# Kernel optimization log

Hardware: AMD Instinct MI355X
Metric: run time of the kernel (lower is better)

## Reference

```python
import jax, jax.numpy as jnp
import numpy as np
import math

B, T, C, H = 2, 2048, 1024, 16
HD = C // H  # head dim = 64

def setup_inputs() -> dict:
    key = jax.random.key(0)
    ks = jax.random.split(key, 12)
    s = 0.02
    return {
        "x": jax.random.normal(ks[0], (B, T, C), dtype=jnp.float32),
        "ln1_g": jnp.ones((C,), jnp.float32),
        "ln1_b": jnp.zeros((C,), jnp.float32),
        "W_attn": jax.random.normal(ks[1], (C, 3 * C), jnp.float32) * s,
        "b_attn": jnp.zeros((3 * C,), jnp.float32),
        "W_ap": jax.random.normal(ks[2], (C, C), jnp.float32) * s,
        "b_ap": jnp.zeros((C,), jnp.float32),
        "ln2_g": jnp.ones((C,), jnp.float32),
        "ln2_b": jnp.zeros((C,), jnp.float32),
        "W_fc": jax.random.normal(ks[3], (C, 4 * C), jnp.float32) * s,
        "b_fc": jnp.zeros((4 * C,), jnp.float32),
        "W_mp": jax.random.normal(ks[4], (4 * C, C), jnp.float32) * s,
        "b_mp": jnp.zeros((C,), jnp.float32),
    }

def layernorm(x, g, b, eps=1e-5):
    mu = jnp.mean(x, axis=-1, keepdims=True)
    var = jnp.mean(jnp.square(x - mu), axis=-1, keepdims=True)
    return (x - mu) * jax.lax.rsqrt(var + eps) * g + b

def gelu_tanh(x):
    # GELU(approximate='tanh')
    c = math.sqrt(2.0 / math.pi)
    return 0.5 * x * (1.0 + jnp.tanh(c * (x + 0.044715 * x * x * x)))

def attention(x, W_attn, b_attn, W_ap, b_ap):
    b, t, c = x.shape
    qkv = x @ W_attn + b_attn                      # [B,T,3C]
    q, k, v = jnp.split(qkv, 3, axis=-1)
    q = q.reshape(b, t, H, HD).transpose(0, 2, 1, 3)  # [B,H,T,hd]
    k = k.reshape(b, t, H, HD).transpose(0, 2, 1, 3)
    v = v.reshape(b, t, H, HD).transpose(0, 2, 1, 3)
    attn = jnp.einsum('bhqd,bhkd->bhqk', q, k) * (1.0 / math.sqrt(HD))
    mask = jnp.tril(jnp.ones((t, t), dtype=bool))
    attn = jnp.where(mask, attn, jnp.float32(-jnp.inf))
    attn = jax.nn.softmax(attn, axis=-1)
    y = jnp.einsum('bhqk,bhkd->bhqd', attn, v)
    y = y.transpose(0, 2, 1, 3).reshape(b, t, c)
    return y @ W_ap + b_ap

def reference(x, ln1_g, ln1_b, W_attn, b_attn, W_ap, b_ap,
              ln2_g, ln2_b, W_fc, b_fc, W_mp, b_mp):
    x = x + attention(layernorm(x, ln1_g, ln1_b), W_attn, b_attn, W_ap, b_ap)
    h = layernorm(x, ln2_g, ln2_b)
    h = gelu_tanh(h @ W_fc + b_fc) @ W_mp + b_mp
    return x + h
```

## Files before the change

kernel.cpp:

```cpp
#include <hip/hip_runtime.h>
#include <stdint.h>

#define TT_ 2048
#define CC_ 1024

typedef unsigned short u16;
typedef __bf16 bf16x8 __attribute__((ext_vector_type(8)));
typedef __bf16 bf16x4 __attribute__((ext_vector_type(4)));
typedef float f32x4 __attribute__((ext_vector_type(4)));
typedef unsigned short u16x8 __attribute__((ext_vector_type(8)));

__device__ __forceinline__ u16 f2bf(float f) {
  unsigned u = __float_as_uint(f);
  u += 0x7fff + ((u >> 16) & 1);
  return (u16)(u >> 16);
}
__device__ __forceinline__ float bf2f(u16 v) {
  return __uint_as_float(((unsigned)v) << 16);
}

__device__ __forceinline__ float gelu_f(float t) {
  float u = 1.5957691216057308f * (t + 0.044715f * t * t * t);
  return t / (1.f + __expf(-u));
}

__device__ __forceinline__ void async_cp16(const u16* g, u16* l) {
  __builtin_amdgcn_global_load_lds(
      (const __attribute__((address_space(1))) void*)(uintptr_t)g,
      (__attribute__((address_space(3))) void*)(uint32_t)(uintptr_t)l,
      16, 0, 0);
}

__device__ __forceinline__ void blockbar() {
  asm volatile("" ::: "memory");
  __builtin_amdgcn_s_barrier();
  asm volatile("" ::: "memory");
}

__global__ __launch_bounds__(256) void kconv_t(const float* __restrict__ W,
                                               u16* __restrict__ WT, int K, int N) {
  __shared__ float t[32][33];
  int n0 = blockIdx.x * 32, k0 = blockIdx.y * 32;
  int tx = threadIdx.x & 31, ty = threadIdx.x >> 5;
#pragma unroll
  for (int r = 0; r < 4; ++r)
    t[ty + 8 * r][tx] = W[(size_t)(k0 + ty + 8 * r) * N + n0 + tx];
  __syncthreads();
#pragma unroll
  for (int r = 0; r < 4; ++r)
    WT[(size_t)(n0 + ty + 8 * r) * K + k0 + tx] = f2bf(t[tx][ty + 8 * r]);
}

__global__ __launch_bounds__(256) void kln(const float* __restrict__ x,
                                           const float* __restrict__ g,
                                           const float* __restrict__ b,
                                           u16* __restrict__ out) {
  int row = blockIdx.x, tid = threadIdx.x;
  const float4* xr = (const float4*)(x + (size_t)row * CC_);
  float4 v = xr[tid];
  float s = v.x + v.y + v.z + v.w;
  float s2 = v.x * v.x + v.y * v.y + v.z * v.z + v.w * v.w;
#pragma unroll
  for (int off = 32; off; off >>= 1) { s += __shfl_down(s, off); s2 += __shfl_down(s2, off); }
  __shared__ float rs[4], rq[4];
  int w = tid >> 6;
  if ((tid & 63) == 0) { rs[w] = s; rq[w] = s2; }
  __syncthreads();
  s = rs[0] + rs[1] + rs[2] + rs[3];
  s2 = rq[0] + rq[1] + rq[2] + rq[3];
  float mean = s * (1.f / CC_);
  float var = s2 * (1.f / CC_) - mean * mean;
  float rstd = rsqrtf(var + 1e-5f);
  float4 gv = ((const float4*)g)[tid];
  float4 bv = ((const float4*)b)[tid];
  u16* orow = out + (size_t)row * CC_ + tid * 4;
  orow[0] = f2bf((v.x - mean) * rstd * gv.x + bv.x);
  orow[1] = f2bf((v.y - mean) * rstd * gv.y + bv.y);
  orow[2] = f2bf((v.z - mean) * rstd * gv.z + bv.z);
  orow[3] = f2bf((v.w - mean) * rstd * gv.w + bv.w);
}

template <int EPI, int NSPLIT>
__global__ __launch_bounds__(256) void kgemm(const u16* __restrict__ A,
                                             const u16* __restrict__ BTm,
                                             const float* __restrict__ bias,
                                             const float* __restrict__ resid,
                                             void* __restrict__ out,
                                             u16* __restrict__ part,
                                             int M, int N, int Ktot,
                                             int chunks_x, int ychunks, int cx) {
  __shared__ __align__(16) u16 As[2][128 * 32];
  __shared__ __align__(16) u16 Bs[2][128 * 32];
  const int tid = threadIdx.x, lane = tid & 63, w = tid >> 6;
  const int llo = lane & 15, lhi = lane >> 4;

  const int bid = blockIdx.x;
  const int xcd = bid & 7, s = bid >> 3;
  const int chx = xcd % chunks_x, chyz = xcd / chunks_x;
  const int z = chyz / ychunks, chy = chyz % ychunks;
  const int bx = chx * cx + s % cx;
  const int cy = (gridDim.x >> 3) / cx;
  const int by = chy * cy + s / cx;

  const int row0 = by * 128, col0 = bx * 128;
  const int wr = w >> 1, wc = w & 1;
  const int crow = lane >> 2;
  const int ck = (lane & 3) * 8;
  const int Kc = Ktot / NSPLIT;
  const int klo = (NSPLIT > 1) ? z * Kc : 0;

  f32x4 acc[4][4] = {};

  auto stage = [&](int bufi, int kof) {
#pragma unroll
    for (int c = w; c < 8; c += 4) {
      int r = c * 16 + crow;
      async_cp16(A + (size_t)(row0 + r) * Ktot + klo + kof + ck, &As[bufi][c * 512]);
      async_cp16(BTm + (size_t)(col0 + r) * Ktot + klo + kof + ck, &Bs[bufi][c * 512]);
    }
  };

  const int nt = Kc / 32;
  stage(0, 0);
  asm volatile("s_waitcnt vmcnt(0)" ::: "memory");
  blockbar();
  int cur = 0;

  for (int t = 0; t < nt; ++t) {
    if (t + 1 < nt) stage(cur ^ 1, (t + 1) * 32);
    bf16x8 af[4], bfr[4];
#pragma unroll
    for (int m = 0; m < 4; ++m)
      af[m] = *(const bf16x8*)&As[cur][(wr * 64 + m * 16 + llo) * 32 + lhi * 8];
#pragma unroll
    for (int n = 0; n < 4; ++n)
      bfr[n] = *(const bf16x8*)&Bs[cur][(wc * 64 + n * 16 + llo) * 32 + lhi * 8];
#pragma unroll
    for (int m = 0; m < 4; ++m)
#pragma unroll
      for (int n = 0; n < 4; ++n)
        acc[m][n] = __builtin_amdgcn_mfma_f32_16x16x32_bf16(af[m], bfr[n], acc[m][n], 0, 0, 0);
    if (t + 1 < nt) {
      asm volatile("s_waitcnt vmcnt(0)" ::: "memory");
      blockbar();
    }
    cur ^= 1;
  }

  const int c_row = row0 + wr * 64 + lhi * 4;
  const int c_col = col0 + wc * 64 + llo;
  const bool fin = (NSPLIT == 1) || (z == 0);
  u16* pb = part + (NSPLIT > 1 ? ((size_t)(z > 0 ? z - 1 : 0)) * M * N : 0);
#pragma unroll
  for (int n = 0; n < 4; ++n) {
    int col = c_col + n * 16;
    float bb = bias[col];
#pragma unroll
    for (int m = 0; m < 4; ++m) {
      f32x4 a = acc[m][n];
#pragma unroll
      for (int i = 0; i < 4; ++i) {
        size_t idx = (size_t)(c_row + m * 16 + i) * N + col;
        if (!fin) {
          pb[idx] = f2bf(a[i]);
        } else {
          float val = a[i] + bb;
          if constexpr (EPI == 1) {
            ((float*)out)[idx] = val + resid[idx];
          } else if constexpr (EPI == 2) {
            ((u16*)out)[idx] = f2bf(gelu_f(val));
          } else {
            ((u16*)out)[idx] = f2bf(val);
          }
        }
      }
    }
  }
}

template <int NP>
__global__ __launch_bounds__(256) void kaddN(float* __restrict__ out,
                                             const u16* __restrict__ p, size_t MN) {
  size_t i0 = ((size_t)blockIdx.x * 256 + threadIdx.x) * 8;
  float4 o0 = *(float4*)(out + i0);
  float4 o1 = *(float4*)(out + i0 + 4);
#pragma unroll
  for (int s = 0; s < NP; ++s) {
    u16x8 v = *(const u16x8*)(p + (size_t)s * MN + i0);
    o0.x += bf2f(v[0]); o0.y += bf2f(v[1]); o0.z += bf2f(v[2]); o0.w += bf2f(v[3]);
    o1.x += bf2f(v[4]); o1.y += bf2f(v[5]); o1.z += bf2f(v[6]); o1.w += bf2f(v[7]);
  }
  *(float4*)(out + i0) = o0;
  *(float4*)(out + i0 + 4) = o1;
}

__global__ __launch_bounds__(256) void kvtrans(const u16* __restrict__ qkv,
                                               u16* __restrict__ VT) {
  int tt = blockIdx.x;
  int bh = blockIdx.y;
  int b = bh >> 4, h = bh & 15;
  __shared__ u16 t[64][72];
  int r = threadIdx.x >> 3, c0 = (threadIdx.x & 7) * 8;
  const u16* src = qkv + (size_t)(b * TT_ + tt * 64) * 3072 + 2048 + h * 64;
#pragma unroll
  for (int it = 0; it < 2; ++it) {
    int rr = r + it * 32;
    *(u16x8*)&t[rr][c0] = *(const u16x8*)(src + (size_t)rr * 3072 + c0);
  }
  __syncthreads();
  u16* dst = VT + ((size_t)bh * 64) * TT_ + tt * 64;
#pragma unroll
  for (int it = 0; it < 2; ++it) {
    int d = r + it * 32;
    u16x8 v;
#pragma unroll
    for (int e = 0; e < 8; ++e) v[e] = t[c0 + e][d];
    *(u16x8*)(dst + (size_t)d * TT_ + c0) = v;
  }
}

__global__ __launch_bounds__(256, 4) void kattn(const u16* __restrict__ qkv,
                                                const u16* __restrict__ VT,
                                                u16* __restrict__ y) {
  const int h = blockIdx.x, b = blockIdx.y, z = blockIdx.z;
  const int tid = threadIdx.x, lane = tid & 63, w = tid >> 6;
  const int llo = lane & 15, lhi = lane >> 4;

  __shared__ __align__(16) u16 Qs[64 * 64];
  __shared__ __align__(16) u16 Ks[2][64 * 64];
  __shared__ __align__(16) u16 Vs[2][64 * 64];
  __shared__ __align__(16) u16 Ps[64 * 72];

  const size_t tok0 = (size_t)b * TT_;
  const u16* qb = qkv + tok0 * 3072 + h * 64;
  const u16* kb = qb + 1024;

  const u16 *kg[2], *vg[2];
#pragma unroll
  for (int it = 0; it < 2; ++it) {
    int p_ = w * 16 + it * 8 + (lane >> 3);
    int krow = ((p_ & 15) << 2) | (p_ >> 4);
    int scol = ((lane & 7) * 8) ^ ((p_ & 7) << 3);
    kg[it] = kb + (size_t)krow * 3072 + scol;
    vg[it] = VT + ((size_t)(b * 16 + h) * 64 + p_) * TT_ + scol;
  }

  auto stageKV = [&](int bufi, int j) {
    async_cp16(kg[0] + (size_t)j * (64 * 3072), &Ks[bufi][(w * 16 + 0) * 64]);
    async_cp16(kg[1] + (size_t)j * (64 * 3072), &Ks[bufi][(w * 16 + 8) * 64]);
    async_cp16(vg[0] + (size_t)j * 64, &Vs[bufi][(w * 16 + 0) * 64]);
    async_cp16(vg[1] + (size_t)j * 64, &Vs[bufi][(w * 16 + 8) * 64]);
  };

  const float alpha = 0.18033688011112042f;
  const int r8 = tid >> 3, ce = (tid & 7) * 8;

#pragma unroll 1
  for (int ph = 0; ph < 2; ++ph) {
    const int qt = ph ? (31 - z) : z;
    const int q0 = qt * 64;

#pragma unroll
    for (int it = 0; it < 2; ++it) {
      int tk = it * 32 + r8;
      u16x8 v = *(const u16x8*)(qb + (size_t)(q0 + tk) * 3072 + ce);
#pragma unroll
      for (int e = 0; e < 8; ++e) v[e] = f2bf(bf2f(v[e]) * alpha);
      *(u16x8*)&Qs[tk * 64 + (ce ^ ((tk & 7) << 3))] = v;
    }
    asm volatile("s_waitcnt lgkmcnt(0)" ::: "memory");
    stageKV(0, 0);
    blockbar();

    bf16x8 aq[2];
#pragma unroll
    for (int kk = 0; kk < 2; ++kk)
      aq[kk] = *(const bf16x8*)&Qs[(w * 16 + llo) * 64 +
                                   ((kk * 32 + lhi * 8) ^ ((llo & 7) << 3))];

    float m_i[4], l_i[4];
    f32x4 o[4] = {};
#pragma unroll
    for (int i = 0; i < 4; ++i) { m_i[i] = -1e30f; l_i[i] = 0.f; }

    int buf = 0;
    for (int j = 0; j <= qt; ++j) {
      if (j < qt) {
        stageKV(buf ^ 1, j + 1);
        asm volatile("s_waitcnt vmcnt(4)" ::: "memory");
      } else {
        asm volatile("s_waitcnt vmcnt(0)" ::: "memory");
      }
      blockbar();

      f32x4 s[4] = {};
      __builtin_amdgcn_s_setprio(1);
#pragma unroll
      for (int nb = 0; nb < 4; ++nb)
#pragma unroll
        for (int kk = 0; kk < 2; ++kk) {
          bf16x8 bk = *(const bf16x8*)&Ks[buf][(nb * 16 + llo) * 64 +
                                              ((kk * 32 + lhi * 8) ^ ((llo & 7) << 3))];
          s[nb] = __builtin_amdgcn_mfma_f32_16x16x32_bf16(aq[kk], bk, s[nb], 0, 0, 0);
        }
      __builtin_amdgcn_s_setprio(0);

      float sc[4][4];
      if (j == qt) {
#pragma unroll
        for (int nb = 0; nb < 4; ++nb)
#pragma unroll
          for (int i = 0; i < 4; ++i) {
            float v = s[nb][i];
            if (llo * 4 + nb > w * 16 + lhi * 4 + i) v = -1e30f;
            sc[nb][i] = v;
          }
      } else {
#pragma unroll
        for (int nb = 0; nb < 4; ++nb)
#pragma unroll
          for (int i = 0; i < 4; ++i) sc[nb][i] = s[nb][i];
      }

      float rm[4];
#pragma unroll
      for (int i = 0; i < 4; ++i) {
        float r = fmaxf(fmaxf(sc[0][i], sc[1][i]), fmaxf(sc[2][i], sc[3][i]));
#pragma unroll
        for (int off = 1; off < 16; off <<= 1) r = fmaxf(r, __shfl_xor(r, off));
        rm[i] = r;
      }

      bool need = (rm[0] > m_i[0] + 8.f) | (rm[1] > m_i[1] + 8.f) |
                  (rm[2] > m_i[2] + 8.f) | (rm[3] > m_i[3] + 8.f);
      if (__any(need)) {
#pragma unroll
        for (int i = 0; i < 4; ++i) {
          float mn = fmaxf(m_i[i], rm[i]);
          float corr = exp2f(m_i[i] - mn);
          l_i[i] *= corr;
#pragma unroll
          for (int db = 0; db < 4; ++db) o[db][i] *= corr;
          m_i[i] = mn;
        }
      }

#pragma unroll
      for (int i = 0; i < 4; ++i) {
        float p0 = exp2f(sc[0][i] - m_i[i]);
        float p1 = exp2f(sc[1][i] - m_i[i]);
        float p2 = exp2f(sc[2][i] - m_i[i]);
        float p3 = exp2f(sc[3][i] - m_i[i]);
        l_i[i] += (p0 + p1) + (p2 + p3);
        bf16x4 pk = {(__bf16)p0, (__bf16)p1, (__bf16)p2, (__bf16)p3};
        *(bf16x4*)&Ps[(w * 16 + lhi * 4 + i) * 72 + llo * 4] = pk;
      }

      bf16x8 pa[2];
#pragma unroll
      for (int kk = 0; kk < 2; ++kk)
        pa[kk] = *(const bf16x8*)&Ps[(w * 16 + llo) * 72 + kk * 32 + lhi * 8];
      __builtin_amdgcn_s_setprio(1);
#pragma unroll
      for (int db = 0; db < 4; ++db)
#pragma unroll
        for (int kk = 0; kk < 2; ++kk) {
          bf16x8 bv = *(const bf16x8*)&Vs[buf][(db * 16 + llo) * 64 +
                                              ((kk * 32 + lhi * 8) ^ ((llo & 7) << 3))];
          o[db] = __builtin_amdgcn_mfma_f32_16x16x32_bf16(pa[kk], bv, o[db], 0, 0, 0);
        }
      __builtin_amdgcn_s_setprio(0);
      blockbar();
      buf ^= 1;
    }

#pragma unroll
    for (int i = 0; i < 4; ++i) {
      float t = l_i[i];
#pragma unroll
      for (int off = 1; off < 16; off <<= 1) t += __shfl_xor(t, off);
      float inv = 1.f / t;
      size_t row = tok0 + q0 + w * 16 + lhi * 4 + i;
#pragma unroll
      for (int db = 0; db < 4; ++db)
        y[row * CC_ + h * 64 + db * 16 + llo] = f2bf(o[db][i] * inv);
    }
  }
}

extern "C" void kernel_launch(void* const* d_in, const int* in_sizes, int n_in,
                              void* d_out, int out_size, void* d_ws, size_t ws_size,
                              hipStream_t stream) {
  (void)in_sizes; (void)n_in; (void)out_size; (void)ws_size;
  const float* x      = (const float*)d_in[0];
  const float* ln1g   = (const float*)d_in[1];
  const float* ln1b   = (const float*)d_in[2];
  const float* W_attn = (const float*)d_in[3];
  const float* b_attn = (const float*)d_in[4];
  const float* W_ap   = (const float*)d_in[5];
  const float* b_ap   = (const float*)d_in[6];
  const float* ln2g   = (const float*)d_in[7];
  const float* ln2b   = (const float*)d_in[8];
  const float* W_fc   = (const float*)d_in[9];
  const float* b_fc   = (const float*)d_in[10];
  const float* W_mp   = (const float*)d_in[11];
  const float* b_mp   = (const float*)d_in[12];

  char* p = (char*)d_ws;
  u16* WTmp   = (u16*)p; p += (size_t)4096 * 1024 * 2;
  u16* WTattn = (u16*)p; p += (size_t)3072 * 1024 * 2;
  u16* WTap   = (u16*)p; p += (size_t)1024 * 1024 * 2;
  u16* WTfc   = (u16*)p; p += (size_t)4096 * 1024 * 2;
  u16* xn     = (u16*)p; p += (size_t)4096 * 1024 * 2;
  u16* qkvb   = (u16*)p; p += (size_t)4096 * 3072 * 2;
  u16* yb     = (u16*)p; p += (size_t)4096 * 1024 * 2;
  float* x1   = (float*)p; p += (size_t)4096 * 1024 * 4;
  u16* h2     = (u16*)p; p += (size_t)4096 * 1024 * 2;
  u16* fcb    = qkvb;
  u16* VT     = (u16*)x1;
  u16* appart = xn;
  u16* mpp    = WTattn;

  kconv_t<<<dim3(96, 32), 256, 0, stream>>>(W_attn, WTattn, 1024, 3072);
  kconv_t<<<dim3(32, 32), 256, 0, stream>>>(W_ap, WTap, 1024, 1024);
  kconv_t<<<dim3(128, 32), 256, 0, stream>>>(W_fc, WTfc, 1024, 4096);
  kconv_t<<<dim3(32, 128), 256, 0, stream>>>(W_mp, WTmp, 4096, 1024);

  kln<<<4096, 256, 0, stream>>>(x, ln1g, ln1b, xn);
  kgemm<0, 1><<<768, 256, 0, stream>>>(xn, WTattn, b_attn, nullptr, qkvb, nullptr,
                                       4096, 3072, 1024, 2, 4, 12);
  kvtrans<<<dim3(32, 32), 256, 0, stream>>>(qkvb, VT);
  kattn<<<dim3(16, 2, 16), 256, 0, stream>>>(qkvb, VT, yb);
  kgemm<1, 2><<<512, 256, 0, stream>>>(yb, WTap, b_ap, x, x1, appart,
                                       4096, 1024, 1024, 1, 4, 8);
  kaddN<1><<<2048, 256, 0, stream>>>(x1, appart, (size_t)4096 * 1024);
  kln<<<4096, 256, 0, stream>>>(x1, ln2g, ln2b, h2);
  kgemm<2, 1><<<1024, 256, 0, stream>>>(h2, WTfc, b_fc, nullptr, fcb, nullptr,
                                        4096, 4096, 1024, 2, 4, 16);
  kgemm<1, 2><<<512, 256, 0, stream>>>(fcb, WTmp, b_mp, x1, (float*)d_out, mpp,
                                       4096, 1024, 4096, 1, 4, 8);
  kaddN<1><<<2048, 256, 0, stream>>>((float*)d_out, mpp, (size_t)4096 * 1024);
}
```

Measured before the change: 282.3 us.

## Add 256x256-tile 8-wave GEMM kernel with staged async loads for large GEMMs

Adds a new GEMM kernel that uses 512 threads and 256x256 output tiles, with double-buffered LDS fed by async global-to-LDS copies. The copies are staged in quarters and interleaved with MFMA phases using explicit vmcnt waits and raised wave priority. The QKV, FC and MLP-projection GEMMs move to this kernel, and the MLP projection now uses a 4-way K split summed by kaddN<3>. Larger tiles raise data reuse and MFMA density, at the cost of fewer blocks (192/256) filling the CUs and more partial-sum traffic for the split-K path.

```diff
diff --git a/kernel.cpp b/kernel.cpp
--- a/kernel.cpp
+++ b/kernel.cpp
@@ -35,6 +35,12 @@
   asm volatile("" ::: "memory");
   __builtin_amdgcn_s_barrier();
   asm volatile("" ::: "memory");
+}
+
+__device__ __forceinline__ void vmw(int n) {
+  if (n >= 4)      asm volatile("s_waitcnt vmcnt(4)" ::: "memory");
+  else if (n >= 2) asm volatile("s_waitcnt vmcnt(2)" ::: "memory");
+  else             asm volatile("s_waitcnt vmcnt(0)" ::: "memory");
 }
 
 __global__ __launch_bounds__(256) void kconv_t(const float* __restrict__ W,
@@ -178,6 +184,174 @@
   }
 }
 
+template <int EPI, int NSPLIT>
+__global__ __launch_bounds__(512, 2) void kgemm8(const u16* __restrict__ A,
+                                                 const u16* __restrict__ BTm,
+                                                 const float* __restrict__ bias,
+                                                 const float* __restrict__ resid,
+                                                 void* __restrict__ out,
+                                                 u16* __restrict__ part,
+                                                 int M, int N, int Ktot,
+                                                 int chunks_x, int ychunks, int cx) {
+  __shared__ __align__(16) u16 LB[65536];
+  const int tid = threadIdx.x, lane = tid & 63, w = tid >> 6;
+  const int llo = lane & 15, lhi = lane >> 4;
+  const int wr = w >> 2, wc = w & 3;
+
+  const int bid = blockIdx.x;
+  const int xcd = bid & 7, s = bid >> 3;
+  const int chx = xcd % chunks_x, chyz = xcd / chunks_x;
+  const int z = chyz / ychunks, chy = chyz % ychunks;
+  const int bx = chx * cx + s % cx;
+  const int cy = (gridDim.x >> 3) / cx;
+  const int by = chy * cy + s / cx;
+
+  const int row0 = by * 256, col0 = bx * 256;
+  const int Kc = Ktot / NSPLIT;
+  const int klo = (NSPLIT > 1) ? z * Kc : 0;
+  const int NT = Kc / 64;
+
+  const int r0 = tid >> 3;
+  const int c0e = ((tid & 7) * 8) ^ (((tid >> 5) & 1) << 4);
+
+  auto STGH = [&](int op, int half, int call, int tt) {
+    u16* d = LB + (tt & 1) * 32768 + op * 16384 + half * 8192 + call * 4096 + w * 512;
+    const u16* src = (op ? BTm : A) +
+                     (size_t)((op ? col0 : row0) + half * 128 + call * 64 + r0) * Ktot +
+                     klo + (size_t)tt * 64 + c0e;
+    async_cp16(src, d);
+  };
+
+  const int swb = (llo & 4) ? 16 : 0;
+  const int ces0 = (lhi * 8) ^ swb;
+  const int ces1 = (32 + lhi * 8) ^ swb;
+  const int abase_off = llo * 64;
+  const int bbase_off = (wc & 1) * 4096 + llo * 64;
+
+  f32x4 acc[8][4] = {};
+
+  STGH(1, 0, 0, 0); STGH(1, 0, 1, 0); STGH(1, 1, 0, 0); STGH(1, 1, 1, 0);
+  STGH(0, 0, 0, 0); STGH(0, 1, 0, 0);
+  STGH(0, 0, 1, 0); STGH(0, 1, 1, 0);
+  vmw(2);
+  blockbar();
+
+  for (int m = 0; m < NT; ++m) {
+    const int slot = m & 1;
+    const bool stg = (m + 1 < NT);
+    const u16* As_ = LB + slot * 32768 + wr * 8192;
+    const u16* Bs_ = LB + slot * 32768 + 16384 + (wc >> 1) * 8192;
+    bf16x8 afA[4][2], bfv[4][2];
+
+#pragma unroll
+    for (int mi = 0; mi < 4; ++mi) {
+      afA[mi][0] = *(const bf16x8*)&As_[mi * 1024 + abase_off + ces0];
+      afA[mi][1] = *(const bf16x8*)&As_[mi * 1024 + abase_off + ces1];
+    }
+#pragma unroll
+    for (int ni = 0; ni < 2; ++ni) {
+      bfv[ni][0] = *(const bf16x8*)&Bs_[ni * 1024 + bbase_off + ces0];
+      bfv[ni][1] = *(const bf16x8*)&Bs_[ni * 1024 + bbase_off + ces1];
+    }
+    if (stg) { STGH(1, 0, 0, m + 1); STGH(1, 0, 1, m + 1); }
+    blockbar();
+    asm volatile("s_waitcnt lgkmcnt(0)" ::: "memory");
+    __builtin_amdgcn_s_setprio(1);
+#pragma unroll
+    for (int ni = 0; ni < 2; ++ni)
+#pragma unroll
+      for (int mi = 0; mi < 4; ++mi)
+#pragma unroll
+        for (int kk = 0; kk < 2; ++kk)
+          acc[mi][ni] = __builtin_amdgcn_mfma_f32_16x16x32_bf16(afA[mi][kk], bfv[ni][kk], acc[mi][ni], 0, 0, 0);
+    __builtin_amdgcn_s_setprio(0);
+    blockbar();
+
+#pragma unroll
+    for (int ni = 2; ni < 4; ++ni) {
+      bfv[ni][0] = *(const bf16x8*)&Bs_[ni * 1024 + bbase_off + ces0];
+      bfv[ni][1] = *(const bf16x8*)&Bs_[ni * 1024 + bbase_off + ces1];
+    }
+    if (stg) { STGH(1, 1, 0, m + 1); STGH(1, 1, 1, m + 1); }
+    blockbar();
+    asm volatile("s_waitcnt lgkmcnt(0)" ::: "memory");
+    __builtin_amdgcn_s_setprio(1);
+#pragma unroll
+    for (int ni = 2; ni < 4; ++ni)
+#pragma unroll
+      for (int mi = 0; mi < 4; ++mi)
+#pragma unroll
+        for (int kk = 0; kk < 2; ++kk)
+          acc[mi][ni] = __builtin_amdgcn_mfma_f32_16x16x32_bf16(afA[mi][kk], bfv[ni][kk], acc[mi][ni], 0, 0, 0);
+    __builtin_amdgcn_s_setprio(0);
+    vmw(stg ? 4 : 0);
+    blockbar();
+
+#pragma unroll
+    for (int mi = 0; mi < 4; ++mi) {
+      afA[mi][0] = *(const bf16x8*)&As_[(4 + mi) * 1024 + abase_off + ces0];
+      afA[mi][1] = *(const bf16x8*)&As_[(4 + mi) * 1024 + abase_off + ces1];
+    }
+    if (stg) { STGH(0, 0, 0, m + 1); STGH(0, 1, 0, m + 1); }
+    blockbar();
+    asm volatile("s_waitcnt lgkmcnt(0)" ::: "memory");
+    __builtin_amdgcn_s_setprio(1);
+#pragma unroll
+    for (int ni = 0; ni < 2; ++ni)
+#pragma unroll
+      for (int mi = 0; mi < 4; ++mi)
+#pragma unroll
+        for (int kk = 0; kk < 2; ++kk)
+          acc[4 + mi][ni] = __builtin_amdgcn_mfma_f32_16x16x32_bf16(afA[mi][kk], bfv[ni][kk], acc[4 + mi][ni], 0, 0, 0);
+    __builtin_amdgcn_s_setprio(0);
+    blockbar();
+
+    if (stg) { STGH(0, 0, 1, m + 1); STGH(0, 1, 1, m + 1); }
+    blockbar();
+    __builtin_amdgcn_s_setprio(1);
+#pragma unroll
+    for (int ni = 2; ni < 4; ++ni)
+#pragma unroll
+      for (int mi = 0; mi < 4; ++mi)
+#pragma unroll
+        for (int kk = 0; kk < 2; ++kk)
+          acc[4 + mi][ni] = __builtin_amdgcn_mfma_f32_16x16x32_bf16(afA[mi][kk], bfv[ni][kk], acc[4 + mi][ni], 0, 0, 0);
+    __builtin_amdgcn_s_setprio(0);
+    if (stg) vmw(2);
+    blockbar();
+  }
+
+  const int c_row0 = row0 + wr * 128 + lhi * 4;
+  const int c_col0 = col0 + wc * 64 + llo;
+  const bool fin = (NSPLIT == 1) || (z == 0);
+  u16* pb = part + (NSPLIT > 1 ? ((size_t)(z > 0 ? z - 1 : 0)) * M * N : 0);
+#pragma unroll
+  for (int n = 0; n < 4; ++n) {
+    int col = c_col0 + n * 16;
+    float bb = bias[col];
+#pragma unroll
+    for (int mm = 0; mm < 8; ++mm) {
+      f32x4 a = acc[mm][n];
+#pragma unroll
+      for (int i = 0; i < 4; ++i) {
+        size_t idx = (size_t)(c_row0 + mm * 16 + i) * N + col;
+        if (!fin) {
+          pb[idx] = f2bf(a[i]);
+        } else {
+          float val = a[i] + bb;
+          if constexpr (EPI == 1) {
+            ((float*)out)[idx] = val + resid[idx];
+          } else if constexpr (EPI == 2) {
+            ((u16*)out)[idx] = f2bf(gelu_f(val));
+          } else {
+            ((u16*)out)[idx] = f2bf(val);
+          }
+        }
+      }
+    }
+  }
+}
+
 template <int NP>
 __global__ __launch_bounds__(256) void kaddN(float* __restrict__ out,
                                              const u16* __restrict__ p, size_t MN) {
@@ -427,17 +601,17 @@
   kconv_t<<<dim3(32, 128), 256, 0, stream>>>(W_mp, WTmp, 4096, 1024);
 
   kln<<<4096, 256, 0, stream>>>(x, ln1g, ln1b, xn);
-  kgemm<0, 1><<<768, 256, 0, stream>>>(xn, WTattn, b_attn, nullptr, qkvb, nullptr,
-                                       4096, 3072, 1024, 2, 4, 12);
+  kgemm8<0, 1><<<192, 512, 0, stream>>>(xn, WTattn, b_attn, nullptr, qkvb, nullptr,
+                                        4096, 3072, 1024, 4, 2, 3);
   kvtrans<<<dim3(32, 32), 256, 0, stream>>>(qkvb, VT);
   kattn<<<dim3(16, 2, 16), 256, 0, stream>>>(qkvb, VT, yb);
   kgemm<1, 2><<<512, 256, 0, stream>>>(yb, WTap, b_ap, x, x1, appart,
                                        4096, 1024, 1024, 1, 4, 8);
   kaddN<1><<<2048, 256, 0, stream>>>(x1, appart, (size_t)4096 * 1024);
   kln<<<4096, 256, 0, stream>>>(x1, ln2g, ln2b, h2);
-  kgemm<2, 1><<<1024, 256, 0, stream>>>(h2, WTfc, b_fc, nullptr, fcb, nullptr,
-                                        4096, 4096, 1024, 2, 4, 16);
-  kgemm<1, 2><<<512, 256, 0, stream>>>(fcb, WTmp, b_mp, x1, (float*)d_out, mpp,
-                                       4096, 1024, 4096, 1, 4, 8);
-  kaddN<1><<<2048, 256, 0, stream>>>((float*)d_out, mpp, (size_t)4096 * 1024);
-}
+  kgemm8<2, 1><<<256, 512, 0, stream>>>(h2, WTfc, b_fc, nullptr, fcb, nullptr,
+                                        4096, 4096, 1024, 2, 4, 8);
+  kgemm8<1, 4><<<256, 512, 0, stream>>>(fcb, WTmp, b_mp, x1, (float*)d_out, mpp,
+                                        4096, 1024, 4096, 1, 2, 4);
+  kaddN<3><<<2048, 256, 0, stream>>>((float*)d_out, mpp, (size_t)4096 * 1024);
+}
```

Result: slower. 312.2 us (+10.6%).

## Fuse V transpose into QKV GEMM epilogue and split-K add into LN2

Applied to the files above, without the earlier changes.

The QKV GEMM epilogue now writes the V columns directly in transposed head-major layout, which removes the separate V-transpose kernel and its extra read and write of V. The residual add of the attention-projection split-K partial is folded into the second layernorm kernel, so the standalone add kernel is dropped. In exchange the V stores from the GEMM are narrower 4-element strided writes, which may coalesce less well.

```diff
diff --git a/kernel.cpp b/kernel.cpp
--- a/kernel.cpp
+++ b/kernel.cpp
@@ -80,6 +80,39 @@
   orow[3] = f2bf((v.w - mean) * rstd * gv.w + bv.w);
 }
 
+__global__ __launch_bounds__(256) void kln2(float* __restrict__ x1,
+                                            const u16* __restrict__ part,
+                                            const float* __restrict__ g,
+                                            const float* __restrict__ b,
+                                            u16* __restrict__ out) {
+  int row = blockIdx.x, tid = threadIdx.x;
+  float4* xr = (float4*)(x1 + (size_t)row * CC_);
+  float4 v = xr[tid];
+  bf16x4 pv = *(const bf16x4*)(part + (size_t)row * CC_ + tid * 4);
+  v.x += (float)pv[0]; v.y += (float)pv[1]; v.z += (float)pv[2]; v.w += (float)pv[3];
+  xr[tid] = v;
+  float s = v.x + v.y + v.z + v.w;
+  float s2 = v.x * v.x + v.y * v.y + v.z * v.z + v.w * v.w;
+#pragma unroll
+  for (int off = 32; off; off >>= 1) { s += __shfl_down(s, off); s2 += __shfl_down(s2, off); }
+  __shared__ float rs[4], rq[4];
+  int w = tid >> 6;
+  if ((tid & 63) == 0) { rs[w] = s; rq[w] = s2; }
+  __syncthreads();
+  s = rs[0] + rs[1] + rs[2] + rs[3];
+  s2 = rq[0] + rq[1] + rq[2] + rq[3];
+  float mean = s * (1.f / CC_);
+  float var = s2 * (1.f / CC_) - mean * mean;
+  float rstd = rsqrtf(var + 1e-5f);
+  float4 gv = ((const float4*)g)[tid];
+  float4 bv = ((const float4*)b)[tid];
+  u16* orow = out + (size_t)row * CC_ + tid * 4;
+  orow[0] = f2bf((v.x - mean) * rstd * gv.x + bv.x);
+  orow[1] = f2bf((v.y - mean) * rstd * gv.y + bv.y);
+  orow[2] = f2bf((v.z - mean) * rstd * gv.z + bv.z);
+  orow[3] = f2bf((v.w - mean) * rstd * gv.w + bv.w);
+}
+
 template <int EPI, int NSPLIT>
 __global__ __launch_bounds__(256) void kgemm(const u16* __restrict__ A,
                                              const u16* __restrict__ BTm,
@@ -151,6 +184,28 @@
   const int c_col = col0 + wc * 64 + llo;
   const bool fin = (NSPLIT == 1) || (z == 0);
   u16* pb = part + (NSPLIT > 1 ? ((size_t)(z > 0 ? z - 1 : 0)) * M * N : 0);
+
+  if constexpr (EPI == 3) {
+    if (col0 >= 2048) {
+      const int b_ = c_row >> 11;
+      const int tokb = c_row & 2047;
+#pragma unroll
+      for (int n = 0; n < 4; ++n) {
+        int col = c_col + n * 16;
+        float bb = bias[col];
+        u16* vrow = part + (size_t)(b_ * 1024 + (col - 2048)) * TT_ + tokb;
+#pragma unroll
+        for (int m = 0; m < 4; ++m) {
+          f32x4 a = acc[m][n];
+          bf16x4 pk = {(__bf16)(a[0] + bb), (__bf16)(a[1] + bb),
+                       (__bf16)(a[2] + bb), (__bf16)(a[3] + bb)};
+          *(bf16x4*)(vrow + m * 16) = pk;
+        }
+      }
+      return;
+    }
+  }
+
 #pragma unroll
   for (int n = 0; n < 4; ++n) {
     int col = c_col + n * 16;
@@ -178,45 +233,16 @@
   }
 }
 
-template <int NP>
-__global__ __launch_bounds__(256) void kaddN(float* __restrict__ out,
-                                             const u16* __restrict__ p, size_t MN) {
+__global__ __launch_bounds__(256) void kadd1(float* __restrict__ out,
+                                             const u16* __restrict__ p) {
   size_t i0 = ((size_t)blockIdx.x * 256 + threadIdx.x) * 8;
   float4 o0 = *(float4*)(out + i0);
   float4 o1 = *(float4*)(out + i0 + 4);
-#pragma unroll
-  for (int s = 0; s < NP; ++s) {
-    u16x8 v = *(const u16x8*)(p + (size_t)s * MN + i0);
-    o0.x += bf2f(v[0]); o0.y += bf2f(v[1]); o0.z += bf2f(v[2]); o0.w += bf2f(v[3]);
-    o1.x += bf2f(v[4]); o1.y += bf2f(v[5]); o1.z += bf2f(v[6]); o1.w += bf2f(v[7]);
-  }
+  u16x8 v = *(const u16x8*)(p + i0);
+  o0.x += bf2f(v[0]); o0.y += bf2f(v[1]); o0.z += bf2f(v[2]); o0.w += bf2f(v[3]);
+  o1.x += bf2f(v[4]); o1.y += bf2f(v[5]); o1.z += bf2f(v[6]); o1.w += bf2f(v[7]);
   *(float4*)(out + i0) = o0;
   *(float4*)(out + i0 + 4) = o1;
-}
-
-__global__ __launch_bounds__(256) void kvtrans(const u16* __restrict__ qkv,
-                                               u16* __restrict__ VT) {
-  int tt = blockIdx.x;
-  int bh = blockIdx.y;
-  int b = bh >> 4, h = bh & 15;
-  __shared__ u16 t[64][72];
-  int r = threadIdx.x >> 3, c0 = (threadIdx.x & 7) * 8;
-  const u16* src = qkv + (size_t)(b * TT_ + tt * 64) * 3072 + 2048 + h * 64;
-#pragma unroll
-  for (int it = 0; it < 2; ++it) {
-    int rr = r + it * 32;
-    *(u16x8*)&t[rr][c0] = *(const u16x8*)(src + (size_t)rr * 3072 + c0);
-  }
-  __syncthreads();
-  u16* dst = VT + ((size_t)bh * 64) * TT_ + tt * 64;
-#pragma unroll
-  for (int it = 0; it < 2; ++it) {
-    int d = r + it * 32;
-    u16x8 v;
-#pragma unroll
-    for (int e = 0; e < 8; ++e) v[e] = t[c0 + e][d];
-    *(u16x8*)(dst + (size_t)d * TT_ + c0) = v;
-  }
 }
 
 __global__ __launch_bounds__(256, 4) void kattn(const u16* __restrict__ qkv,
@@ -427,17 +453,15 @@
   kconv_t<<<dim3(32, 128), 256, 0, stream>>>(W_mp, WTmp, 4096, 1024);
 
   kln<<<4096, 256, 0, stream>>>(x, ln1g, ln1b, xn);
-  kgemm<0, 1><<<768, 256, 0, stream>>>(xn, WTattn, b_attn, nullptr, qkvb, nullptr,
+  kgemm<3, 1><<<768, 256, 0, stream>>>(xn, WTattn, b_attn, nullptr, qkvb, VT,
                                        4096, 3072, 1024, 2, 4, 12);
-  kvtrans<<<dim3(32, 32), 256, 0, stream>>>(qkvb, VT);
   kattn<<<dim3(16, 2, 16), 256, 0, stream>>>(qkvb, VT, yb);
   kgemm<1, 2><<<512, 256, 0, stream>>>(yb, WTap, b_ap, x, x1, appart,
                                        4096, 1024, 1024, 1, 4, 8);
-  kaddN<1><<<2048, 256, 0, stream>>>(x1, appart, (size_t)4096 * 1024);
-  kln<<<4096, 256, 0, stream>>>(x1, ln2g, ln2b, h2);
+  kln2<<<4096, 256, 0, stream>>>(x1, appart, ln2g, ln2b, h2);
   kgemm<2, 1><<<1024, 256, 0, stream>>>(h2, WTfc, b_fc, nullptr, fcb, nullptr,
                                         4096, 4096, 1024, 2, 4, 16);
   kgemm<1, 2><<<512, 256, 0, stream>>>(fcb, WTmp, b_mp, x1, (float*)d_out, mpp,
                                        4096, 1024, 4096, 1, 4, 8);
-  kaddN<1><<<2048, 256, 0, stream>>>((float*)d_out, mpp, (size_t)4096 * 1024);
-}
+  kadd1<<<2048, 256, 0, stream>>>((float*)d_out, mpp);
+}
```

New measurement: 280.7 us. About the same (-0.6%).
